# Kernel tuning notes

Measured on AMD Instinct MI355X. Metric: run time of the kernel, lower is better.

Reference implementation:

```python
import jax, jax.numpy as jnp
import numpy as np

B, T, C = 4, 2048, 2048
N_HEAD = 16
HEAD_DIM = C // N_HEAD


def setup_inputs() -> dict:
    key = jax.random.key(0)
    k1, k2, k3, k4, k5 = jax.random.split(key, 5)
    s = 1.0 / np.sqrt(C)
    return {
        "x": jax.random.normal(k1, (B, T, C), dtype=jnp.float32),
        "w_attn": jax.random.normal(k2, (C, 3 * C), dtype=jnp.float32) * s,
        "b_attn": jax.random.normal(k3, (3 * C,), dtype=jnp.float32) * 0.02,
        "w_proj": jax.random.normal(k4, (C, C), dtype=jnp.float32) * s,
        "b_proj": jax.random.normal(k5, (C,), dtype=jnp.float32) * 0.02,
    }


def reference(x, w_attn, b_attn, w_proj, b_proj):
    Bsz, Tlen, Cdim = x.shape
    # fused QKV projection
    qkv = x @ w_attn + b_attn  # [B,T,3C]
    q, k, v = jnp.split(qkv, 3, axis=-1)
    # [B,T,C] -> [B,H,T,D]
    def heads(t):
        return t.reshape(Bsz, Tlen, N_HEAD, HEAD_DIM).transpose(0, 2, 1, 3)
    q, k, v = heads(q), heads(k), heads(v)
    scale = 1.0 / np.sqrt(HEAD_DIM).astype(np.float32)
    att = jnp.einsum("bhqd,bhkd->bhqk", q, k) * scale  # [B,H,T,T]
    causal = jnp.tril(jnp.ones((Tlen, Tlen), dtype=bool))
    att = jnp.where(causal, att, -jnp.inf)
    att = jax.nn.softmax(att, axis=-1)
    y = jnp.einsum("bhqk,bhkd->bhqd", att, v)  # [B,H,T,D]
    y = y.transpose(0, 2, 1, 3).reshape(Bsz, Tlen, Cdim)
    return y @ w_proj + b_proj
```

## Files before the change

kernel.cpp:

```cpp
#include <hip/hip_runtime.h>

typedef __bf16 bf16x8 __attribute__((ext_vector_type(8)));
typedef __bf16 bf16x4 __attribute__((ext_vector_type(4)));
typedef float  f32x4  __attribute__((ext_vector_type(4)));
typedef float  f32x16 __attribute__((ext_vector_type(16)));
typedef unsigned u32x4 __attribute__((ext_vector_type(4)));

#define LOG2E 1.4426950408889634f

__device__ __forceinline__ void gload16(const void* g, void* l) {
  __builtin_amdgcn_global_load_lds((const __attribute__((address_space(1))) void*)g,
                                   (__attribute__((address_space(3))) void*)l, 16, 0, 0);
}

__device__ __forceinline__ unsigned pk(float lo, float hi) {
  unsigned short lu = __builtin_bit_cast(unsigned short, (__bf16)lo);
  unsigned short hu = __builtin_bit_cast(unsigned short, (__bf16)hi);
  return (unsigned)lu | ((unsigned)hu << 16);
}

__global__ __launch_bounds__(256) void cvt4(const float* __restrict__ in,
                                            __bf16* __restrict__ outp, int n4) {
  int i = blockIdx.x * blockDim.x + threadIdx.x;
  if (i < n4) {
    float4 v = ((const float4*)in)[i];
    bf16x4 o = { (__bf16)v.x, (__bf16)v.y, (__bf16)v.z, (__bf16)v.w };
    *(bf16x4*)(outp + (size_t)i * 4) = o;
  }
}

__global__ __launch_bounds__(256) void transcvt(const float* __restrict__ w,
                                                __bf16* __restrict__ wt,
                                                int K, int N) {
  __shared__ float tile[32][33];
  const int n0 = blockIdx.x * 32, k0 = blockIdx.y * 32;
  const int tx = threadIdx.x, ty = threadIdx.y;
#pragma unroll
  for (int i = 0; i < 4; ++i)
    tile[ty + i * 8][tx] = w[(size_t)(k0 + ty + i * 8) * N + n0 + tx];
  __syncthreads();
#pragma unroll
  for (int i = 0; i < 4; ++i)
    wt[(size_t)(n0 + ty + i * 8) * K + k0 + tx] = (__bf16)tile[tx][ty + i * 8];
}

template <int EPI, int NCOLS>
__global__ __launch_bounds__(512, 2)
void gemm_bt(const __bf16* __restrict__ A, const __bf16* __restrict__ Bt,
             const float* __restrict__ bias,
             __bf16* __restrict__ Qb, __bf16* __restrict__ Kb,
             __bf16* __restrict__ Vtb, float* __restrict__ Out) {
  constexpr int K = 2048;
  constexpr int NSTEP = K / 32;
  constexpr int NBX = NCOLS / 256;
  __shared__ __align__(16) __bf16 lds_[65536];
  __bf16* const As_ = lds_;
  __bf16* const Bs_ = lds_ + 32768;
  const int tid = threadIdx.x, lane = tid & 63, w = tid >> 6;
  const int wr = w >> 2, wc = w & 3;
  const int l15 = lane & 15, g = lane >> 4;

  const int nwg = (int)gridDim.x;
  const int flat = ((int)blockIdx.x & 7) * (nwg >> 3) + ((int)blockIdx.x >> 3);
  const int by = flat / NBX, bx = flat % NBX;

  const __bf16* Ab = A + (size_t)by * 256 * K;
  const __bf16* Bb = Bt + (size_t)bx * 256 * K;

  const int gsw = (((tid & 3) ^ ((tid >> 3) & 3)) * 8);
  const __bf16* srcA[2];
  const __bf16* srcB[2];
#pragma unroll
  for (int c = 0; c < 2; ++c) {
    const int idx = c * 512 + tid;
    const int row = idx >> 2;
    srcA[c] = Ab + (size_t)row * K + gsw;
    srcB[c] = Bb + (size_t)row * K + gsw;
  }
  const int ldst = tid * 8;

  const int csw = ((g ^ ((l15 >> 1) & 3)) * 8);
  const int aoff = (wr * 128 + l15) * 32 + csw;
  const int boff = (wc * 64 + l15) * 32 + csw;

  f32x4 acc[8][4] = {};

#define LDA(rs, i) (*(const bf16x8*)(As_ + (rs) + aoff + (i) * 512))
#define LDB(rs, i) (*(const bf16x8*)(Bs_ + (rs) + boff + (i) * 512))
#define ISSUE_A(jj) { const int s_ = ((jj) & 3) * 8192;                       \
    gload16(srcA[0] + (size_t)(jj) * 32, (void*)(As_ + s_ + ldst));           \
    gload16(srcA[1] + (size_t)(jj) * 32, (void*)(As_ + s_ + 4096 + ldst)); }
#define ISSUE_B(jj) { const int s_ = ((jj) & 3) * 8192;                       \
    gload16(srcB[0] + (size_t)(jj) * 32, (void*)(Bs_ + s_ + ldst));           \
    gload16(srcB[1] + (size_t)(jj) * 32, (void*)(Bs_ + s_ + 4096 + ldst)); }
#define VM8 asm volatile("s_waitcnt vmcnt(8)" ::: "memory")
#define VM4 asm volatile("s_waitcnt vmcnt(4)" ::: "memory")
#define VM0 asm volatile("s_waitcnt vmcnt(0)" ::: "memory")
#define VMN
#define MFMA8(p0, p1, bq, m0, m1)                                             \
  _Pragma("unroll")                                                           \
  for (int ni = 0; ni < 4; ++ni) {                                            \
    acc[m0][ni] = __builtin_amdgcn_mfma_f32_16x16x32_bf16(p0, bq[ni],         \
                                                          acc[m0][ni], 0,0,0);\
    acc[m1][ni] = __builtin_amdgcn_mfma_f32_16x16x32_bf16(p1, bq[ni],         \
                                                          acc[m1][ni], 0,0,0);\
  }

#define KSTEP(j, ISS, VMW, RB, avC, avN, bvC, bvN) {                          \
    const int rs_ = ((j) & 3) * 8192;                                         \
    const int rn_ = (((j) + 1) & 3) * 8192;                                   \
    bf16x8 a2 = LDA(rs_, 2), a3 = LDA(rs_, 3);                                \
    MFMA8(avC[0], avC[1], bvC, 0, 1);                                         \
    bf16x8 a4 = LDA(rs_, 4), a5 = LDA(rs_, 5);                                \
    MFMA8(a2, a3, bvC, 2, 3);                                                 \
    if (ISS) ISSUE_A((j) + 3);                                                \
    bf16x8 a6 = LDA(rs_, 6), a7 = LDA(rs_, 7);                                \
    MFMA8(a4, a5, bvC, 4, 5);                                                 \
    if (ISS) ISSUE_B((j) + 3);                                                \
    VMW;                                                                      \
    __builtin_amdgcn_s_barrier();                                             \
    if (RB) {                                                                 \
      avN[0] = LDA(rn_, 0); avN[1] = LDA(rn_, 1);                             \
      bvN[0] = LDB(rn_, 0); bvN[1] = LDB(rn_, 1);                             \
      bvN[2] = LDB(rn_, 2); bvN[3] = LDB(rn_, 3);                             \
    }                                                                         \
    MFMA8(a6, a7, bvC, 6, 7);                                                 \
    __builtin_amdgcn_s_barrier();                                             \
  }

  bf16x8 avX[2], avY[2], bvX[4], bvY[4];

  ISSUE_A(0); ISSUE_B(0);
  ISSUE_A(1); ISSUE_B(1);
  ISSUE_A(2); ISSUE_B(2);
  VM8;
  __builtin_amdgcn_s_barrier();
  avX[0] = LDA(0, 0); avX[1] = LDA(0, 1);
  bvX[0] = LDB(0, 0); bvX[1] = LDB(0, 1);
  bvX[2] = LDB(0, 2); bvX[3] = LDB(0, 3);

  for (int j = 0; j < NSTEP - 4; j += 2) {
    KSTEP(j,     true, VM8, true, avX, avY, bvX, bvY);
    KSTEP(j + 1, true, VM8, true, avY, avX, bvY, bvX);
  }
  KSTEP(NSTEP - 4, true,  VM8, true,  avX, avY, bvX, bvY);
  KSTEP(NSTEP - 3, false, VM4, true,  avY, avX, bvY, bvX);
  KSTEP(NSTEP - 2, false, VM0, true,  avX, avY, bvX, bvY);
  KSTEP(NSTEP - 1, false, VMN, false, avY, avX, bvY, bvX);

#undef KSTEP
#undef MFMA8
#undef ISSUE_A
#undef ISSUE_B
#undef LDA
#undef LDB

  const int r0 = by * 256 + wr * 128 + (g << 2);
  const int c0 = bx * 256 + wc * 64 + l15;
#pragma unroll
  for (int ni = 0; ni < 4; ++ni) {
    const int c = c0 + ni * 16;
    const float bvs = bias[c];
    if constexpr (EPI == 0) {
      const int sel = c >> 11, cc = c & 2047, h = cc >> 7, d = cc & 127;
#pragma unroll
      for (int mi = 0; mi < 8; ++mi) {
        const int r = r0 + mi * 16;
        const int bb = r >> 11, t = r & 2047;
        if (sel == 2) {
          bf16x4 pv;
#pragma unroll
          for (int j = 0; j < 4; ++j) pv[j] = (__bf16)(acc[mi][ni][j] + bvs);
          *(bf16x4*)(Vtb + ((size_t)(bb * 16 + h) * 128 + d) * 2048 + t) = pv;
        } else {
          __bf16* dst = (sel == 0 ? Qb : Kb) + ((size_t)(bb * 16 + h) * 2048 + t) * 128 + d;
          const float sc = (sel == 0) ? 0.08838834764831845f : 1.0f;
#pragma unroll
          for (int j = 0; j < 4; ++j)
            dst[(size_t)j * 128] = (__bf16)((acc[mi][ni][j] + bvs) * sc);
        }
      }
    } else {
#pragma unroll
      for (int mi = 0; mi < 8; ++mi) {
        const int r = r0 + mi * 16;
#pragma unroll
        for (int j = 0; j < 4; ++j)
          Out[(size_t)(r + j) * NCOLS + c] = acc[mi][ni][j] + bvs;
      }
    }
  }
}

__global__ __launch_bounds__(512, 2)
void attn_fwd(const __bf16* __restrict__ Qb, const __bf16* __restrict__ Kb,
              const __bf16* __restrict__ Vtb, __bf16* __restrict__ Yb) {
  __shared__ __align__(16) char lds[65536];
  const int tid = threadIdx.x;
  const int lane = tid & 63, w = tid >> 6;
  const int l31 = lane & 31, hi = lane >> 5;
  const int kx = (l31 & 7) << 4;

  const int G = (int)gridDim.x;
  for (int rr = 0;; ++rr) {
    const int pos = (rr & 1) ? (G - 1 - (int)blockIdx.x) : (int)blockIdx.x;
    const int item = rr * G + pos;
    if (item >= 512) break;
    const int qb = 7 - (item >> 6);
    const int bh = item & 63;
    const int bidx = bh >> 4, h = bh & 15;
    const int nt = (qb + 1) * 4;

    const __bf16* Qh = Qb + ((size_t)bh * 2048 + qb * 256) * 128;
    const __bf16* Kh = Kb + (size_t)bh * 2048 * 128;
    const __bf16* Vh = Vtb + (size_t)bh * 128 * 2048;

    bf16x8 qf[8];
    {
      const __bf16* qrow = Qh + (size_t)(w * 32 + l31) * 128 + hi * 8;
#pragma unroll
      for (int ds = 0; ds < 8; ++ds) qf[ds] = *(const bf16x8*)(qrow + ds * 16);
    }

    {
      uint4 kr[2], vr[2];
#pragma unroll
      for (int c = 0; c < 2; ++c) {
        const int idx = c * 512 + tid;
        kr[c] = *(const uint4*)(Kh + (size_t)(idx >> 4) * 128 + (idx & 15) * 8);
        vr[c] = *(const uint4*)(Vh + (size_t)(idx >> 3) * 2048 + (idx & 7) * 8);
      }
      __syncthreads();
      char* K0 = lds;
      char* V0 = lds + 16384;
#pragma unroll
      for (int c = 0; c < 2; ++c) {
        const int idx = c * 512 + tid;
        { const int row = idx >> 4, colB = (idx & 15) * 16;
          *(uint4*)(K0 + row * 256 + (colB ^ ((row & 7) << 4))) = kr[c]; }
        { const int row = idx >> 3, colB = (idx & 7) * 16;
          *(uint4*)(V0 + row * 128 + (colB ^ ((row & 7) << 4))) = vr[c]; }
      }
      __syncthreads();
    }

    f32x16 accO[4] = {};
    float mL = -3.0e38f, lsum = 0.f;
    const int qg  = qb * 256 + w * 32 + l31;
    const int qwb = qb * 256 + w * 32;

    for (int t = 0; t < nt; ++t) {
      const int kv0 = t * 64;
      char* Kc = lds + (t & 1) * 32768;
      char* Vc = Kc + 16384;
      const bool pf = (t + 1 < nt);
      uint4 kr[2], vr[2];
      if (pf) {
        const int kvn = kv0 + 64;
#pragma unroll
        for (int c = 0; c < 2; ++c) {
          const int idx = c * 512 + tid;
          kr[c] = *(const uint4*)(Kh + (size_t)(kvn + (idx >> 4)) * 128 + (idx & 15) * 8);
          vr[c] = *(const uint4*)(Vh + (size_t)(idx >> 3) * 2048 + kvn + (idx & 7) * 8);
        }
      }

      f32x16 s0 = {}, s1 = {};
      __builtin_amdgcn_s_setprio(1);
#pragma unroll
      for (int ds = 0; ds < 8; ++ds) {
        const int cb = (ds * 32 + hi * 16) ^ kx;
        bf16x8 k0 = *(const bf16x8*)(Kc + l31 * 256 + cb);
        bf16x8 k1 = *(const bf16x8*)(Kc + (32 + l31) * 256 + cb);
        s0 = __builtin_amdgcn_mfma_f32_32x32x16_bf16(k0, qf[ds], s0, 0, 0, 0);
        s1 = __builtin_amdgcn_mfma_f32_32x32x16_bf16(k1, qf[ds], s1, 0, 0, 0);
      }
      __builtin_amdgcn_s_setprio(0);

      f32x16 a0, a1;
#pragma unroll
      for (int r = 0; r < 16; ++r) { a0[r] = s0[r] * LOG2E; a1[r] = s1[r] * LOG2E; }
      if (kv0 + 63 > qwb) {
#pragma unroll
        for (int r = 0; r < 16; ++r) {
          const int kvr = kv0 + (r & 3) + 8 * (r >> 2) + 4 * hi;
          if (kvr > qg)      a0[r] = -1.0e38f;
          if (kvr + 32 > qg) a1[r] = -1.0e38f;
        }
      }

      float pm = a0[0];
#pragma unroll
      for (int r = 1; r < 16; ++r) pm = fmaxf(pm, a0[r]);
#pragma unroll
      for (int r = 0; r < 16; ++r) pm = fmaxf(pm, a1[r]);
      pm = fmaxf(pm, __shfl_xor(pm, 32, 64));

      if (!__all(pm - mL <= 11.5f)) {
        const float mn = fmaxf(mL, pm);
        const float corr = exp2f(mL - mn);
        mL = mn;
        lsum *= corr;
#pragma unroll
        for (int db = 0; db < 4; ++db)
#pragma unroll
          for (int r = 0; r < 16; ++r) accO[db][r] *= corr;
      }

      float p[32];
      float rs = 0.f;
#pragma unroll
      for (int r = 0; r < 16; ++r) { p[r] = exp2f(a0[r] - mL); rs += p[r]; }
#pragma unroll
      for (int r = 0; r < 16; ++r) { p[16 + r] = exp2f(a1[r] - mL); rs += p[16 + r]; }
      rs += __shfl_xor(rs, 32, 64);
      lsum += rs;

      bf16x8 pa[4];
#pragma unroll
      for (int f = 0; f < 2; ++f) {
        unsigned wv[8];
#pragma unroll
        for (int i = 0; i < 8; ++i)
          wv[i] = pk(p[f * 16 + 2 * i], p[f * 16 + 2 * i + 1]);
        const unsigned x0 = (unsigned)__shfl_xor((int)(hi ? wv[0] : wv[2]), 32, 64);
        const unsigned x1 = (unsigned)__shfl_xor((int)(hi ? wv[1] : wv[3]), 32, 64);
        const unsigned x2 = (unsigned)__shfl_xor((int)(hi ? wv[4] : wv[6]), 32, 64);
        const unsigned x3 = (unsigned)__shfl_xor((int)(hi ? wv[5] : wv[7]), 32, 64);
        u32x4 A, B;
        A[0] = hi ? x0 : wv[0];  A[1] = hi ? x1 : wv[1];
        A[2] = hi ? wv[2] : x0;  A[3] = hi ? wv[3] : x1;
        B[0] = hi ? x2 : wv[4];  B[1] = hi ? x3 : wv[5];
        B[2] = hi ? wv[6] : x2;  B[3] = hi ? wv[7] : x3;
        pa[f * 2 + 0] = __builtin_bit_cast(bf16x8, A);
        pa[f * 2 + 1] = __builtin_bit_cast(bf16x8, B);
      }

      __builtin_amdgcn_s_setprio(1);
#pragma unroll
      for (int ks = 0; ks < 4; ++ks) {
        const int cb = (ks * 32 + hi * 16) ^ kx;
#pragma unroll
        for (int db = 0; db < 4; ++db) {
          bf16x8 vf = *(const bf16x8*)(Vc + (db * 32 + l31) * 128 + cb);
          accO[db] = __builtin_amdgcn_mfma_f32_32x32x16_bf16(vf, pa[ks], accO[db], 0, 0, 0);
        }
      }
      __builtin_amdgcn_s_setprio(0);

      if (pf) {
        char* Kn = lds + ((t + 1) & 1) * 32768;
        char* Vn = Kn + 16384;
#pragma unroll
        for (int c = 0; c < 2; ++c) {
          const int idx = c * 512 + tid;
          { const int row = idx >> 4, colB = (idx & 15) * 16;
            *(uint4*)(Kn + row * 256 + (colB ^ ((row & 7) << 4))) = kr[c]; }
          { const int row = idx >> 3, colB = (idx & 7) * 16;
            *(uint4*)(Vn + row * 128 + (colB ^ ((row & 7) << 4))) = vr[c]; }
        }
      }
      __syncthreads();
    }

    const float rl = 1.0f / lsum;
    __bf16* Yw = Yb + ((size_t)bidx * 2048 + qg) * 2048 + h * 128;
#pragma unroll
    for (int db = 0; db < 4; ++db)
#pragma unroll
      for (int j = 0; j < 4; ++j) {
        bf16x4 o;
#pragma unroll
        for (int i = 0; i < 4; ++i) o[i] = (__bf16)(accO[db][4 * j + i] * rl);
        *(bf16x4*)(Yw + db * 32 + 8 * j + 4 * hi) = o;
      }
  }
}

extern "C" void kernel_launch(void* const* d_in, const int* in_sizes, int n_in,
                              void* d_out, int out_size, void* d_ws, size_t ws_size,
                              hipStream_t stream) {
  const float* x      = (const float*)d_in[0];
  const float* w_attn = (const float*)d_in[1];
  const float* b_attn = (const float*)d_in[2];
  const float* w_proj = (const float*)d_in[3];
  const float* b_proj = (const float*)d_in[4];
  float* out = (float*)d_out;

  __bf16* Qb  = (__bf16*)d_ws;
  __bf16* Kb  = Qb  + (size_t)16777216;
  __bf16* Vtb = Kb  + (size_t)16777216;
  __bf16* XYb = Vtb + (size_t)16777216;
  __bf16* Wt  = XYb + (size_t)16777216;

  cvt4<<<dim3(16384), dim3(256), 0, stream>>>(x, XYb, 4194304);
  transcvt<<<dim3(192, 64), dim3(32, 8), 0, stream>>>(w_attn, Wt, 2048, 6144);
  gemm_bt<0, 6144><<<dim3(768), dim3(512), 0, stream>>>(XYb, Wt, b_attn,
                                                        Qb, Kb, Vtb, nullptr);
  transcvt<<<dim3(64, 64), dim3(32, 8), 0, stream>>>(w_proj, Wt, 2048, 2048);
  attn_fwd<<<dim3(256), dim3(512), 0, stream>>>(Qb, Kb, Vtb, XYb);
  gemm_bt<1, 2048><<<dim3(256), dim3(512), 0, stream>>>(XYb, Wt, b_proj,
                                                        nullptr, nullptr, nullptr, out);
}
```

Before: 472.7 us.

## Stream K/V tiles into LDS asynchronously in 128-wide double-buffered chunks

Replaces the register-staged K/V prefetch with direct global-to-LDS DMA loads (global_load_lds), with the XOR swizzle applied on the global source address. Each pipeline stage now covers 128 keys, processed as two 64-key sub-steps, and waits on vmcnt so one stage's loads overlap the previous stage's compute. This halves the barriers per key and removes the VGPR round trip. The log2(e) factor is folded into the Q scaling in the QKV epilogue, so the per-element multiply in attention goes away. The cost is 128 KB of LDS per block, which likely permits only one 512-thread block per CU instead of the two the launch bounds request.

```diff
diff --git a/kernel.cpp b/kernel.cpp
--- a/kernel.cpp
+++ b/kernel.cpp
@@ -174,7 +174,8 @@
           *(bf16x4*)(Vtb + ((size_t)(bb * 16 + h) * 128 + d) * 2048 + t) = pv;
         } else {
           __bf16* dst = (sel == 0 ? Qb : Kb) + ((size_t)(bb * 16 + h) * 2048 + t) * 128 + d;
-          const float sc = (sel == 0) ? 0.08838834764831845f : 1.0f;
+          const float sc = (sel == 0)
+              ? (0.08838834764831845f * 1.4426950408889634f) : 1.0f;
 #pragma unroll
           for (int j = 0; j < 4; ++j)
             dst[(size_t)j * 128] = (__bf16)((acc[mi][ni][j] + bvs) * sc);
@@ -195,11 +196,15 @@
 __global__ __launch_bounds__(512, 2)
 void attn_fwd(const __bf16* __restrict__ Qb, const __bf16* __restrict__ Kb,
               const __bf16* __restrict__ Vtb, __bf16* __restrict__ Yb) {
-  __shared__ __align__(16) char lds[65536];
+  __shared__ __align__(16) char lds[131072];
   const int tid = threadIdx.x;
   const int lane = tid & 63, w = tid >> 6;
   const int l31 = lane & 31, hi = lane >> 5;
-  const int kx = (l31 & 7) << 4;
+  const int kxn = (l31 & 15) << 4;
+
+  const int rowb = tid >> 4;
+  const int ch8  = (((tid & 15) ^ (rowb & 15)) * 8);
+  const int dsto = tid * 16;
 
   const int G = (int)gridDim.x;
   for (int rr = 0;; ++rr) {
@@ -209,39 +214,30 @@
     const int qb = 7 - (item >> 6);
     const int bh = item & 63;
     const int bidx = bh >> 4, h = bh & 15;
-    const int nt = (qb + 1) * 4;
+    const int nt2 = (qb + 1) * 2;
 
     const __bf16* Qh = Qb + ((size_t)bh * 2048 + qb * 256) * 128;
     const __bf16* Kh = Kb + (size_t)bh * 2048 * 128;
     const __bf16* Vh = Vtb + (size_t)bh * 128 * 2048;
+    const __bf16* pKs = Kh + rowb * 128 + ch8;
+    const __bf16* pVs = Vh + (size_t)rowb * 2048 + ch8;
+
+#define ISSUEW(tw) { char* bp_ = lds + ((tw) & 1) * 65536;                    \
+    _Pragma("unroll")                                                         \
+    for (int i_ = 0; i_ < 4; ++i_) {                                          \
+      gload16(pKs + (size_t)(tw) * 16384 + i_ * 4096,                         \
+              bp_ + i_ * 8192 + dsto);                                        \
+      gload16(pVs + (size_t)(tw) * 128 + (size_t)i_ * 65536,                  \
+              bp_ + 32768 + i_ * 8192 + dsto);                                \
+    } }
+
+    ISSUEW(0);
 
     bf16x8 qf[8];
     {
       const __bf16* qrow = Qh + (size_t)(w * 32 + l31) * 128 + hi * 8;
 #pragma unroll
       for (int ds = 0; ds < 8; ++ds) qf[ds] = *(const bf16x8*)(qrow + ds * 16);
-    }
-
-    {
-      uint4 kr[2], vr[2];
-#pragma unroll
-      for (int c = 0; c < 2; ++c) {
-        const int idx = c * 512 + tid;
-        kr[c] = *(const uint4*)(Kh + (size_t)(idx >> 4) * 128 + (idx & 15) * 8);
-        vr[c] = *(const uint4*)(Vh + (size_t)(idx >> 3) * 2048 + (idx & 7) * 8);
-      }
-      __syncthreads();
-      char* K0 = lds;
-      char* V0 = lds + 16384;
-#pragma unroll
-      for (int c = 0; c < 2; ++c) {
-        const int idx = c * 512 + tid;
-        { const int row = idx >> 4, colB = (idx & 15) * 16;
-          *(uint4*)(K0 + row * 256 + (colB ^ ((row & 7) << 4))) = kr[c]; }
-        { const int row = idx >> 3, colB = (idx & 7) * 16;
-          *(uint4*)(V0 + row * 128 + (colB ^ ((row & 7) << 4))) = vr[c]; }
-      }
-      __syncthreads();
     }
 
     f32x16 accO[4] = {};
@@ -249,119 +245,106 @@
     const int qg  = qb * 256 + w * 32 + l31;
     const int qwb = qb * 256 + w * 32;
 
-    for (int t = 0; t < nt; ++t) {
-      const int kv0 = t * 64;
-      char* Kc = lds + (t & 1) * 32768;
-      char* Vc = Kc + 16384;
-      const bool pf = (t + 1 < nt);
-      uint4 kr[2], vr[2];
-      if (pf) {
-        const int kvn = kv0 + 64;
-#pragma unroll
-        for (int c = 0; c < 2; ++c) {
-          const int idx = c * 512 + tid;
-          kr[c] = *(const uint4*)(Kh + (size_t)(kvn + (idx >> 4)) * 128 + (idx & 15) * 8);
-          vr[c] = *(const uint4*)(Vh + (size_t)(idx >> 3) * 2048 + kvn + (idx & 7) * 8);
-        }
-      }
-
-      f32x16 s0 = {}, s1 = {};
-      __builtin_amdgcn_s_setprio(1);
-#pragma unroll
-      for (int ds = 0; ds < 8; ++ds) {
-        const int cb = (ds * 32 + hi * 16) ^ kx;
-        bf16x8 k0 = *(const bf16x8*)(Kc + l31 * 256 + cb);
-        bf16x8 k1 = *(const bf16x8*)(Kc + (32 + l31) * 256 + cb);
-        s0 = __builtin_amdgcn_mfma_f32_32x32x16_bf16(k0, qf[ds], s0, 0, 0, 0);
-        s1 = __builtin_amdgcn_mfma_f32_32x32x16_bf16(k1, qf[ds], s1, 0, 0, 0);
-      }
-      __builtin_amdgcn_s_setprio(0);
-
-      f32x16 a0, a1;
-#pragma unroll
-      for (int r = 0; r < 16; ++r) { a0[r] = s0[r] * LOG2E; a1[r] = s1[r] * LOG2E; }
-      if (kv0 + 63 > qwb) {
-#pragma unroll
-        for (int r = 0; r < 16; ++r) {
-          const int kvr = kv0 + (r & 3) + 8 * (r >> 2) + 4 * hi;
-          if (kvr > qg)      a0[r] = -1.0e38f;
-          if (kvr + 32 > qg) a1[r] = -1.0e38f;
-        }
-      }
-
-      float pm = a0[0];
-#pragma unroll
-      for (int r = 1; r < 16; ++r) pm = fmaxf(pm, a0[r]);
-#pragma unroll
-      for (int r = 0; r < 16; ++r) pm = fmaxf(pm, a1[r]);
-      pm = fmaxf(pm, __shfl_xor(pm, 32, 64));
-
-      if (!__all(pm - mL <= 11.5f)) {
-        const float mn = fmaxf(mL, pm);
-        const float corr = exp2f(mL - mn);
-        mL = mn;
-        lsum *= corr;
-#pragma unroll
-        for (int db = 0; db < 4; ++db)
-#pragma unroll
-          for (int r = 0; r < 16; ++r) accO[db][r] *= corr;
-      }
-
-      float p[32];
-      float rs = 0.f;
-#pragma unroll
-      for (int r = 0; r < 16; ++r) { p[r] = exp2f(a0[r] - mL); rs += p[r]; }
-#pragma unroll
-      for (int r = 0; r < 16; ++r) { p[16 + r] = exp2f(a1[r] - mL); rs += p[16 + r]; }
-      rs += __shfl_xor(rs, 32, 64);
-      lsum += rs;
-
-      bf16x8 pa[4];
-#pragma unroll
-      for (int f = 0; f < 2; ++f) {
-        unsigned wv[8];
-#pragma unroll
-        for (int i = 0; i < 8; ++i)
-          wv[i] = pk(p[f * 16 + 2 * i], p[f * 16 + 2 * i + 1]);
-        const unsigned x0 = (unsigned)__shfl_xor((int)(hi ? wv[0] : wv[2]), 32, 64);
-        const unsigned x1 = (unsigned)__shfl_xor((int)(hi ? wv[1] : wv[3]), 32, 64);
-        const unsigned x2 = (unsigned)__shfl_xor((int)(hi ? wv[4] : wv[6]), 32, 64);
-        const unsigned x3 = (unsigned)__shfl_xor((int)(hi ? wv[5] : wv[7]), 32, 64);
-        u32x4 A, B;
-        A[0] = hi ? x0 : wv[0];  A[1] = hi ? x1 : wv[1];
-        A[2] = hi ? wv[2] : x0;  A[3] = hi ? wv[3] : x1;
-        B[0] = hi ? x2 : wv[4];  B[1] = hi ? x3 : wv[5];
-        B[2] = hi ? wv[6] : x2;  B[3] = hi ? wv[7] : x3;
-        pa[f * 2 + 0] = __builtin_bit_cast(bf16x8, A);
-        pa[f * 2 + 1] = __builtin_bit_cast(bf16x8, B);
-      }
-
-      __builtin_amdgcn_s_setprio(1);
-#pragma unroll
-      for (int ks = 0; ks < 4; ++ks) {
-        const int cb = (ks * 32 + hi * 16) ^ kx;
-#pragma unroll
-        for (int db = 0; db < 4; ++db) {
-          bf16x8 vf = *(const bf16x8*)(Vc + (db * 32 + l31) * 128 + cb);
-          accO[db] = __builtin_amdgcn_mfma_f32_32x32x16_bf16(vf, pa[ks], accO[db], 0, 0, 0);
-        }
-      }
-      __builtin_amdgcn_s_setprio(0);
-
-      if (pf) {
-        char* Kn = lds + ((t + 1) & 1) * 32768;
-        char* Vn = Kn + 16384;
-#pragma unroll
-        for (int c = 0; c < 2; ++c) {
-          const int idx = c * 512 + tid;
-          { const int row = idx >> 4, colB = (idx & 15) * 16;
-            *(uint4*)(Kn + row * 256 + (colB ^ ((row & 7) << 4))) = kr[c]; }
-          { const int row = idx >> 3, colB = (idx & 7) * 16;
-            *(uint4*)(Vn + row * 128 + (colB ^ ((row & 7) << 4))) = vr[c]; }
-        }
-      }
-      __syncthreads();
+    for (int t2 = 0; t2 < nt2; ++t2) {
+      char* Kc = lds + (t2 & 1) * 65536;
+      char* Vc = Kc + 32768;
+      if (t2 + 1 < nt2) {
+        ISSUEW(t2 + 1);
+        asm volatile("s_waitcnt vmcnt(8)" ::: "memory");
+      } else {
+        asm volatile("s_waitcnt vmcnt(0)" ::: "memory");
+      }
+      __builtin_amdgcn_s_barrier();
+
+#pragma unroll
+      for (int s = 0; s < 2; ++s) {
+        const int kv0 = t2 * 128 + s * 64;
+        const char* Ks = Kc + s * 16384;
+
+        f32x16 s0 = {}, s1 = {};
+        __builtin_amdgcn_s_setprio(1);
+#pragma unroll
+        for (int ds = 0; ds < 8; ++ds) {
+          const int cb = (ds * 32 + hi * 16) ^ kxn;
+          bf16x8 k0 = *(const bf16x8*)(Ks + l31 * 256 + cb);
+          bf16x8 k1 = *(const bf16x8*)(Ks + (32 + l31) * 256 + cb);
+          s0 = __builtin_amdgcn_mfma_f32_32x32x16_bf16(k0, qf[ds], s0, 0, 0, 0);
+          s1 = __builtin_amdgcn_mfma_f32_32x32x16_bf16(k1, qf[ds], s1, 0, 0, 0);
+        }
+        __builtin_amdgcn_s_setprio(0);
+
+        if (kv0 + 63 > qwb) {
+#pragma unroll
+          for (int r = 0; r < 16; ++r) {
+            const int kvr = kv0 + (r & 3) + 8 * (r >> 2) + 4 * hi;
+            if (kvr > qg)      s0[r] = -1.0e38f;
+            if (kvr + 32 > qg) s1[r] = -1.0e38f;
+          }
+        }
+
+        float pm = s0[0];
+#pragma unroll
+        for (int r = 1; r < 16; ++r) pm = fmaxf(pm, s0[r]);
+#pragma unroll
+        for (int r = 0; r < 16; ++r) pm = fmaxf(pm, s1[r]);
+        pm = fmaxf(pm, __shfl_xor(pm, 32, 64));
+
+        if (!__all(pm - mL <= 11.5f)) {
+          const float mn = fmaxf(mL, pm);
+          const float corr = exp2f(mL - mn);
+          mL = mn;
+          lsum *= corr;
+#pragma unroll
+          for (int db = 0; db < 4; ++db)
+#pragma unroll
+            for (int r = 0; r < 16; ++r) accO[db][r] *= corr;
+        }
+
+        float p[32];
+        float rs = 0.f;
+#pragma unroll
+        for (int r = 0; r < 16; ++r) { p[r] = exp2f(s0[r] - mL); rs += p[r]; }
+#pragma unroll
+        for (int r = 0; r < 16; ++r) { p[16 + r] = exp2f(s1[r] - mL); rs += p[16 + r]; }
+        rs += __shfl_xor(rs, 32, 64);
+        lsum += rs;
+
+        bf16x8 pa[4];
+#pragma unroll
+        for (int f = 0; f < 2; ++f) {
+          unsigned wv[8];
+#pragma unroll
+          for (int i = 0; i < 8; ++i)
+            wv[i] = pk(p[f * 16 + 2 * i], p[f * 16 + 2 * i + 1]);
+          const unsigned x0 = (unsigned)__shfl_xor((int)(hi ? wv[0] : wv[2]), 32, 64);
+          const unsigned x1 = (unsigned)__shfl_xor((int)(hi ? wv[1] : wv[3]), 32, 64);
+          const unsigned x2 = (unsigned)__shfl_xor((int)(hi ? wv[4] : wv[6]), 32, 64);
+          const unsigned x3 = (unsigned)__shfl_xor((int)(hi ? wv[5] : wv[7]), 32, 64);
+          u32x4 A, B;
+          A[0] = hi ? x0 : wv[0];  A[1] = hi ? x1 : wv[1];
+          A[2] = hi ? wv[2] : x0;  A[3] = hi ? wv[3] : x1;
+          B[0] = hi ? x2 : wv[4];  B[1] = hi ? x3 : wv[5];
+          B[2] = hi ? wv[6] : x2;  B[3] = hi ? wv[7] : x3;
+          pa[f * 2 + 0] = __builtin_bit_cast(bf16x8, A);
+          pa[f * 2 + 1] = __builtin_bit_cast(bf16x8, B);
+        }
+
+        __builtin_amdgcn_s_setprio(1);
+#pragma unroll
+        for (int ks = 0; ks < 4; ++ks) {
+          const int cb = (s * 128 + ks * 32 + hi * 16) ^ kxn;
+#pragma unroll
+          for (int db = 0; db < 4; ++db) {
+            bf16x8 vf = *(const bf16x8*)(Vc + (db * 32 + l31) * 256 + cb);
+            accO[db] = __builtin_amdgcn_mfma_f32_32x32x16_bf16(vf, pa[ks],
+                                                               accO[db], 0, 0, 0);
+          }
+        }
+        __builtin_amdgcn_s_setprio(0);
+      }
+      __builtin_amdgcn_s_barrier();
     }
+#undef ISSUEW
 
     const float rl = 1.0f / lsum;
     __bf16* Yw = Yb + ((size_t)bidx * 2048 + qg) * 2048 + h * 128;
```

After: 413.8 us. 12.5% less time.
